# Kernel tuning notes

Hardware: AMD Instinct MI355X
Metric: run time of the kernel (lower is better)

Reference implementation:

```python
import jax, jax.numpy as jnp
import numpy as np

N_NODES = 100000


def gcn_conv(x, src, dst, W, b):
    # PyG GCNConv: add self-loops, symmetric norm D^-1/2 (A+I) D^-1/2, then linear.
    n = x.shape[0]
    xw = x @ W  # [N, out]
    deg = jax.ops.segment_sum(jnp.ones_like(dst, dtype=xw.dtype), dst, num_segments=n)
    dinv = jnp.where(deg > 0, jax.lax.rsqrt(deg), 0.0)
    norm = dinv[src] * dinv[dst]  # [E_total]
    out = jax.ops.segment_sum(norm[:, None] * xw[src], dst, num_segments=n)
    return out + b


def setup_inputs() -> dict:
    key = jax.random.key(0)
    k1, k2, k3, k4, k5, k6 = jax.random.split(key, 6)
    d = 64
    E = 1600000
    x = jax.random.normal(k1, (N_NODES, d), dtype=jnp.float32)
    edge_index = jax.random.randint(k2, (2, E), 0, N_NODES, dtype=jnp.int64)
    s = 1.0 / np.sqrt(d)
    W1 = jax.random.normal(k3, (d, d), dtype=jnp.float32) * s
    b1 = jax.random.normal(k4, (d,), dtype=jnp.float32) * 0.01
    W2 = jax.random.normal(k5, (d, d), dtype=jnp.float32) * s
    b2 = jax.random.normal(k6, (d,), dtype=jnp.float32) * 0.01
    return {"x": x, "edge_index": edge_index, "W1": W1, "b1": b1, "W2": W2, "b2": b2}


def reference(x, edge_index, W1, b1, W2, b2):
    n = x.shape[0]
    loops = jnp.arange(n, dtype=edge_index.dtype)
    src = jnp.concatenate([edge_index[0], loops])
    dst = jnp.concatenate([edge_index[1], loops])
    out = jax.nn.relu(gcn_conv(x, src, dst, W1, b1))
    out = gcn_conv(out, src, dst, W2, b2)
    return jax.nn.relu(out + x)
```

## Files before the change

kernel.cpp:

```cpp
#include <hip/hip_runtime.h>

constexpr int BIN_CHUNK = 2048;
constexpr int BK_SHIFT  = 9;
constexpr int BK_NODES  = 1 << BK_SHIFT;
constexpr int CAP       = 10240;

static __device__ __forceinline__ float4 mkf4(float x, float y, float z, float w) {
  float4 r; r.x = x; r.y = y; r.z = z; r.w = w; return r;
}

static __device__ __forceinline__ unsigned pack_bf16(float a, float b) {
  unsigned ua = __float_as_uint(a); ua = (ua + 0x7fffu + ((ua >> 16) & 1u)) >> 16;
  unsigned ub = __float_as_uint(b); ub = (ub + 0x7fffu + ((ub >> 16) & 1u)) >> 16;
  return ua | (ub << 16);
}
static __device__ __forceinline__ float blo(unsigned v) { return __uint_as_float(v << 16); }
static __device__ __forceinline__ float bhi(unsigned v) { return __uint_as_float(v & 0xffff0000u); }


__global__ void k_zero256(int* __restrict__ p) { p[threadIdx.x] = 0; }


__global__ __launch_bounds__(256) void k_bin(const int* __restrict__ src,
                                             const int* __restrict__ dst,
                                             int* __restrict__ bcur,
                                             int* __restrict__ binned, int E) {
  __shared__ int lh[4][256];
  __shared__ int cbase[4][256];
  const int tid = threadIdx.x, wv = tid >> 6, lane = tid & 63;
  for (int i = lane; i < 256; i += 64) lh[wv][i] = 0;
  __syncthreads();

  const int e0 = blockIdx.x * BIN_CHUNK;
  const int e1 = min(e0 + BIN_CHUNK, E);
  const int q  = BIN_CHUNK / 4;
  const int we0 = min(e0 + wv * q, e1);
  const int we1 = min(we0 + q, e1);

  for (int e = we0 + lane; e < we1; e += 64)
    atomicAdd(&lh[wv][dst[e] >> BK_SHIFT], 1);
  __syncthreads();

  {
    const int b = tid;
    int c0 = lh[0][b], c1 = lh[1][b], c2 = lh[2][b], c3 = lh[3][b];
    int tot = c0 + c1 + c2 + c3;
    int base = tot ? atomicAdd(bcur + b, tot) : 0;
    cbase[0][b] = base;
    cbase[1][b] = base + c0;
    cbase[2][b] = base + c0 + c1;
    cbase[3][b] = base + c0 + c1 + c2;
    lh[0][b] = 0; lh[1][b] = 0; lh[2][b] = 0; lh[3][b] = 0;
  }
  __syncthreads();

  for (int e = we0 + lane; e < we1; e += 64) {
    int d = dst[e];
    int b = d >> BK_SHIFT;
    int pos = cbase[wv][b] + atomicAdd(&lh[wv][b], 1);
    if (pos < CAP)
      binned[b * CAP + pos] = src[e] | ((d & (BK_NODES - 1)) << 17);
  }
}


__global__ __launch_bounds__(256) void k_place3(const int* __restrict__ bcur,
                                                const int* __restrict__ binned,
                                                int2* __restrict__ nfo,
                                                float* __restrict__ dinv,
                                                int* __restrict__ col, int N) {
  __shared__ int lhw[4][BK_NODES];
  __shared__ int lplace[CAP];
  __shared__ int wsum[4];
  const int tid = threadIdx.x, lane = tid & 63, wv = tid >> 6;
  const int b = blockIdx.x;
  const int nb0 = b << BK_SHIFT;
  const int base = b * CAP;
  const int len = min(bcur[b], CAP);

  for (int i = tid; i < 4 * BK_NODES; i += 256) ((int*)lhw)[i] = 0;
  __syncthreads();

  const int q = (len + 3) >> 2;
  const int we0 = min(wv * q, len);
  const int we1 = min(we0 + q, len);

  for (int e = we0 + lane; e < we1; e += 64)
    atomicAdd(&lhw[wv][binned[base + e] >> 17], 1);
  __syncthreads();

  const int i0 = 2 * tid, i1 = 2 * tid + 1;
  const int c0 = lhw[0][i0] + lhw[1][i0] + lhw[2][i0] + lhw[3][i0];
  const int c1 = lhw[0][i1] + lhw[1][i1] + lhw[2][i1] + lhw[3][i1];
  const int tot = c0 + c1;
  int t = tot;
#pragma unroll
  for (int o = 1; o < 64; o <<= 1) { int n = __shfl_up(t, o); if (lane >= o) t += n; }
  if (lane == 63) wsum[wv] = t;
  __syncthreads();
  int wbase = 0;
#pragma unroll
  for (int w = 0; w < 3; ++w) if (w < wv) wbase += wsum[w];
  const int excl = wbase + t - tot;

  const int n0 = nb0 + i0, n1 = nb0 + i1;
  if (n0 < N) {
    int2 s; s.x = base + excl; s.y = base + excl + c0;
    nfo[n0] = s; dinv[n0] = rsqrtf((float)(c0 + 1));
  }
  if (n1 < N) {
    int2 s; s.x = base + excl + c0; s.y = base + excl + c0 + c1;
    nfo[n1] = s; dinv[n1] = rsqrtf((float)(c1 + 1));
  }

  int run = excl;
#pragma unroll
  for (int w = 0; w < 4; ++w) { int tmp = lhw[w][i0]; lhw[w][i0] = run; run += tmp; }
#pragma unroll
  for (int w = 0; w < 4; ++w) { int tmp = lhw[w][i1]; lhw[w][i1] = run; run += tmp; }
  __syncthreads();

  for (int e = we0 + lane; e < we1; e += 64) {
    int v = binned[base + e];
    int pos = atomicAdd(&lhw[wv][v >> 17], 1);
    lplace[pos] = v & 0x1FFFF;
  }
  __syncthreads();
  for (int e = tid; e < len; e += 256) col[base + e] = lplace[e];
}


__global__ __launch_bounds__(256) void k_gemmf(const float* __restrict__ X,
                                               const float* __restrict__ W,
                                               const float* __restrict__ dinv,
                                               unsigned* __restrict__ Y, int N) {
  __shared__ float4 Wl[1024];
  const int tid = threadIdx.x;
  const float4* __restrict__ W4 = (const float4*)W;
#pragma unroll
  for (int i = 0; i < 4; ++i) Wl[tid + i * 256] = W4[tid + i * 256];
  __syncthreads();

  const int rg = tid >> 4, cq = tid & 15;
  const int row0 = blockIdx.x * 64 + rg * 4;
  const float4* __restrict__ X4 = (const float4*)X;

  int ridx[4];
#pragma unroll
  for (int r = 0; r < 4; ++r) ridx[r] = min(row0 + r, N - 1);

  float4 acc[4];
#pragma unroll
  for (int r = 0; r < 4; ++r) acc[r] = mkf4(0.f, 0.f, 0.f, 0.f);

#pragma unroll 4
  for (int k4 = 0; k4 < 16; ++k4) {
    float4 xv[4];
#pragma unroll
    for (int r = 0; r < 4; ++r) xv[r] = X4[(size_t)ridx[r] * 16 + k4];
#pragma unroll
    for (int kk = 0; kk < 4; ++kk) {
      const float4 w = Wl[(k4 * 4 + kk) * 16 + cq];
#pragma unroll
      for (int r = 0; r < 4; ++r) {
        const float xk = (kk == 0) ? xv[r].x : (kk == 1) ? xv[r].y
                        : (kk == 2) ? xv[r].z : xv[r].w;
        acc[r].x = fmaf(xk, w.x, acc[r].x);
        acc[r].y = fmaf(xk, w.y, acc[r].y);
        acc[r].z = fmaf(xk, w.z, acc[r].z);
        acc[r].w = fmaf(xk, w.w, acc[r].w);
      }
    }
  }

#pragma unroll
  for (int r = 0; r < 4; ++r) {
    const int row = row0 + r;
    if (row < N) {
      const float di = dinv[row];
      uint2 o;
      o.x = pack_bf16(di * acc[r].x, di * acc[r].y);
      o.y = pack_bf16(di * acc[r].z, di * acc[r].w);
      *(uint2*)(Y + (size_t)row * 32 + cq * 2) = o;
    }
  }
}


__global__ __launch_bounds__(256) void k_gemmb(const uint4* __restrict__ X4,
                                               const float* __restrict__ W,
                                               const float* __restrict__ dinv,
                                               unsigned* __restrict__ Y, int N) {
  __shared__ float4 Wl[1024];
  const int tid = threadIdx.x;
  const float4* __restrict__ W4 = (const float4*)W;
#pragma unroll
  for (int i = 0; i < 4; ++i) Wl[tid + i * 256] = W4[tid + i * 256];
  __syncthreads();

  const int rg = tid >> 4, cq = tid & 15;
  const int row0 = blockIdx.x * 64 + rg * 4;

  int ridx[4];
#pragma unroll
  for (int r = 0; r < 4; ++r) ridx[r] = min(row0 + r, N - 1);

  float4 acc[4];
#pragma unroll
  for (int r = 0; r < 4; ++r) acc[r] = mkf4(0.f, 0.f, 0.f, 0.f);

#pragma unroll 2
  for (int k8 = 0; k8 < 8; ++k8) {
    uint4 xv[4];
#pragma unroll
    for (int r = 0; r < 4; ++r) xv[r] = X4[(size_t)ridx[r] * 8 + k8];
#pragma unroll
    for (int kk = 0; kk < 8; ++kk) {
      const float4 w = Wl[(k8 * 8 + kk) * 16 + cq];
#pragma unroll
      for (int r = 0; r < 4; ++r) {
        const unsigned d = (kk < 2) ? xv[r].x : (kk < 4) ? xv[r].y
                          : (kk < 6) ? xv[r].z : xv[r].w;
        const float xk = (kk & 1) ? bhi(d) : blo(d);
        acc[r].x = fmaf(xk, w.x, acc[r].x);
        acc[r].y = fmaf(xk, w.y, acc[r].y);
        acc[r].z = fmaf(xk, w.z, acc[r].z);
        acc[r].w = fmaf(xk, w.w, acc[r].w);
      }
    }
  }

#pragma unroll
  for (int r = 0; r < 4; ++r) {
    const int row = row0 + r;
    if (row < N) {
      const float di = dinv[row];
      uint2 o;
      o.x = pack_bf16(di * acc[r].x, di * acc[r].y);
      o.y = pack_bf16(di * acc[r].z, di * acc[r].w);
      *(uint2*)(Y + (size_t)row * 32 + cq * 2) = o;
    }
  }
}


template <int MODE>
__global__ __launch_bounds__(256) void k_gather(const int2* __restrict__ nfo,
                                                const int* __restrict__ col,
                                                const float* __restrict__ dinv,
                                                const uint2* __restrict__ xws2,
                                                const float4* __restrict__ b4,
                                                const float4* __restrict__ x4,
                                                void* __restrict__ outp, int N) {
  const int node = blockIdx.x * 4 + (threadIdx.x >> 6);
  if (node >= N) return;
  const int lane = threadIdx.x & 63;
  const int sub = lane >> 4;
  const int lg = lane & 15;

  const int2 se = nfo[node];
  const uint2 sv = xws2[(size_t)node * 16 + lg];
  const float di = dinv[node];
  const float4 bb = b4[lg];
  float4 xx = mkf4(0.f, 0.f, 0.f, 0.f);
  if (MODE == 2) xx = x4[(size_t)node * 16 + lg];

  const int s0 = se.x;
  const int deg = se.y - se.x;
  const int dcap = min(deg, 64);

  int cv = 0;
  if (deg > 0) cv = col[min(s0 + lane, s0 + deg - 1)];

  float a0 = 0.f, a1 = 0.f, a2 = 0.f, a3 = 0.f;

  int jb = 0;
  for (; jb + 16 <= dcap; jb += 16) {
    int c0 = __shfl(cv, jb + sub);
    int c1 = __shfl(cv, jb + 4 + sub);
    int c2 = __shfl(cv, jb + 8 + sub);
    int c3 = __shfl(cv, jb + 12 + sub);
    uint2 v0 = xws2[(size_t)c0 * 16 + lg];
    uint2 v1 = xws2[(size_t)c1 * 16 + lg];
    uint2 v2 = xws2[(size_t)c2 * 16 + lg];
    uint2 v3 = xws2[(size_t)c3 * 16 + lg];
    a0 += (blo(v0.x) + blo(v1.x)) + (blo(v2.x) + blo(v3.x));
    a1 += (bhi(v0.x) + bhi(v1.x)) + (bhi(v2.x) + bhi(v3.x));
    a2 += (blo(v0.y) + blo(v1.y)) + (blo(v2.y) + blo(v3.y));
    a3 += (bhi(v0.y) + bhi(v1.y)) + (bhi(v2.y) + bhi(v3.y));
  }
  if (jb < dcap) {
    const int j0 = jb + sub, j1 = jb + 4 + sub, j2 = jb + 8 + sub, j3 = jb + 12 + sub;
    const int m = dcap - 1;
    int c0 = __shfl(cv, min(j0, m));
    int c1 = __shfl(cv, min(j1, m));
    int c2 = __shfl(cv, min(j2, m));
    int c3 = __shfl(cv, min(j3, m));
    uint2 v0 = xws2[(size_t)c0 * 16 + lg];
    uint2 v1 = xws2[(size_t)c1 * 16 + lg];
    uint2 v2 = xws2[(size_t)c2 * 16 + lg];
    uint2 v3 = xws2[(size_t)c3 * 16 + lg];
    a0 += (j0 < dcap ? blo(v0.x) : 0.f) + (j1 < dcap ? blo(v1.x) : 0.f)
        + (j2 < dcap ? blo(v2.x) : 0.f) + (j3 < dcap ? blo(v3.x) : 0.f);
    a1 += (j0 < dcap ? bhi(v0.x) : 0.f) + (j1 < dcap ? bhi(v1.x) : 0.f)
        + (j2 < dcap ? bhi(v2.x) : 0.f) + (j3 < dcap ? bhi(v3.x) : 0.f);
    a2 += (j0 < dcap ? blo(v0.y) : 0.f) + (j1 < dcap ? blo(v1.y) : 0.f)
        + (j2 < dcap ? blo(v2.y) : 0.f) + (j3 < dcap ? blo(v3.y) : 0.f);
    a3 += (j0 < dcap ? bhi(v0.y) : 0.f) + (j1 < dcap ? bhi(v1.y) : 0.f)
        + (j2 < dcap ? bhi(v2.y) : 0.f) + (j3 < dcap ? bhi(v3.y) : 0.f);
  }
  for (int e = s0 + 64 + sub; e < s0 + deg; e += 4) {
    uint2 v = xws2[(size_t)col[e] * 16 + lg];
    a0 += blo(v.x); a1 += bhi(v.x); a2 += blo(v.y); a3 += bhi(v.y);
  }

  a0 += __shfl_xor(a0, 16); a1 += __shfl_xor(a1, 16);
  a2 += __shfl_xor(a2, 16); a3 += __shfl_xor(a3, 16);
  a0 += __shfl_xor(a0, 32); a1 += __shfl_xor(a1, 32);
  a2 += __shfl_xor(a2, 32); a3 += __shfl_xor(a3, 32);

  if (sub == 0) {
    a0 += blo(sv.x); a1 += bhi(sv.x); a2 += blo(sv.y); a3 += bhi(sv.y);
    float r0 = fmaf(di, a0, bb.x);
    float r1 = fmaf(di, a1, bb.y);
    float r2 = fmaf(di, a2, bb.z);
    float r3 = fmaf(di, a3, bb.w);
    if (MODE == 2) {
      r0 += xx.x; r1 += xx.y; r2 += xx.z; r3 += xx.w;
      ((float4*)outp)[(size_t)node * 16 + lg] =
          mkf4(fmaxf(r0, 0.f), fmaxf(r1, 0.f), fmaxf(r2, 0.f), fmaxf(r3, 0.f));
    } else {
      uint2 o;
      o.x = pack_bf16(fmaxf(r0, 0.f), fmaxf(r1, 0.f));
      o.y = pack_bf16(fmaxf(r2, 0.f), fmaxf(r3, 0.f));
      ((uint2*)outp)[(size_t)node * 16 + lg] = o;
    }
  }
}


extern "C" void kernel_launch(void* const* d_in, const int* in_sizes, int n_in,
                              void* d_out, int out_size, void* d_ws, size_t ws_size,
                              hipStream_t stream) {
  const float* x  = (const float*)d_in[0];
  const int*   ei = (const int*)d_in[1];
  const float* W1 = (const float*)d_in[2];
  const float* b1 = (const float*)d_in[3];
  const float* W2 = (const float*)d_in[4];
  const float* b2 = (const float*)d_in[5];
  float* out = (float*)d_out;

  const int N = in_sizes[0] / 64;
  const int E = in_sizes[1] / 2;
  const int NB = (N + BK_NODES - 1) >> BK_SHIFT;

  const int* srcp = ei;
  const int* dstp = ei + E;

  auto align = [](size_t v) { return (v + 255) & ~(size_t)255; };
  char* ws = (char*)d_ws;
  size_t o = 0;
  int2* nfo   = (int2*)(ws + o); o = align(o + (size_t)N * 8);
  float* dinv = (float*)(ws + o); o = align(o + (size_t)N * 4);
  int* bcur   = (int*)(ws + o); o = align(o + 256 * 4);
  int* col    = (int*)(ws + o); o = align(o + (size_t)NB * CAP * 4);
  unsigned* xws = (unsigned*)(ws + o); o = align(o + (size_t)N * 128);
  unsigned* h1  = (unsigned*)(ws + o); o = align(o + (size_t)N * 128);
  int* binned = (int*)h1;

  const int bGm  = (N + 63) / 64;
  const int bG   = (N + 3) / 4;
  const int bBin = (E + BIN_CHUNK - 1) / BIN_CHUNK;

  k_zero256<<<1, 256, 0, stream>>>(bcur);
  k_bin<<<bBin, 256, 0, stream>>>(srcp, dstp, bcur, binned, E);
  k_place3<<<NB, 256, 0, stream>>>(bcur, binned, nfo, dinv, col, N);

  k_gemmf<<<bGm, 256, 0, stream>>>(x, W1, dinv, xws, N);
  k_gather<1><<<bG, 256, 0, stream>>>(nfo, col, dinv, (const uint2*)xws,
                                      (const float4*)b1, (const float4*)x,
                                      (void*)h1, N);

  k_gemmb<<<bGm, 256, 0, stream>>>((const uint4*)h1, W2, dinv, xws, N);
  k_gather<2><<<bG, 256, 0, stream>>>(nfo, col, dinv, (const uint2*)xws,
                                      (const float4*)b2, (const float4*)x,
                                      (void*)out, N);
}
```

Measured before the change: 173.1 us.

## Halve bucket size, vectorize binning loads, packed-float gather accumulation

Buckets shrink from 512 to 256 nodes (CAP 5120, up to 512 buckets), so k_place3 launches twice as many blocks with one node per thread and a smaller LDS footprint, which should raise occupancy. k_bin reads dst/src as int4 when the chunk is full and aligned, the col copy-out uses int4 stores, and the gather accumulates bf16 pairs in 2-wide float vectors to encourage packed FP32 adds. The smaller CAP leaves less headroom for skewed bucket sizes, and more buckets raises contention on the global bucket counters.

```diff
diff --git a/kernel.cpp b/kernel.cpp
--- a/kernel.cpp
+++ b/kernel.cpp
@@ -1,9 +1,12 @@
 #include <hip/hip_runtime.h>
 
 constexpr int BIN_CHUNK = 2048;
-constexpr int BK_SHIFT  = 9;
+constexpr int BK_SHIFT  = 8;
 constexpr int BK_NODES  = 1 << BK_SHIFT;
-constexpr int CAP       = 10240;
+constexpr int NBMAX     = 512;
+constexpr int CAP       = 5120;
+
+typedef float v2f __attribute__((ext_vector_type(2)));
 
 static __device__ __forceinline__ float4 mkf4(float x, float y, float z, float w) {
   float4 r; r.x = x; r.y = y; r.z = z; r.w = w; return r;
@@ -16,19 +19,22 @@
 }
 static __device__ __forceinline__ float blo(unsigned v) { return __uint_as_float(v << 16); }
 static __device__ __forceinline__ float bhi(unsigned v) { return __uint_as_float(v & 0xffff0000u); }
-
-
-__global__ void k_zero256(int* __restrict__ p) { p[threadIdx.x] = 0; }
+static __device__ __forceinline__ v2f bpair(unsigned v) {
+  v2f p; p.x = blo(v); p.y = bhi(v); return p;
+}
+
+
+__global__ void k_zero(int* __restrict__ p) { p[threadIdx.x] = 0; }
 
 
 __global__ __launch_bounds__(256) void k_bin(const int* __restrict__ src,
                                              const int* __restrict__ dst,
                                              int* __restrict__ bcur,
                                              int* __restrict__ binned, int E) {
-  __shared__ int lh[4][256];
-  __shared__ int cbase[4][256];
+  __shared__ int lh[4][NBMAX];
+  __shared__ int cbase[4][NBMAX];
   const int tid = threadIdx.x, wv = tid >> 6, lane = tid & 63;
-  for (int i = lane; i < 256; i += 64) lh[wv][i] = 0;
+  for (int i = lane; i < NBMAX; i += 64) lh[wv][i] = 0;
   __syncthreads();
 
   const int e0 = blockIdx.x * BIN_CHUNK;
@@ -36,13 +42,26 @@
   const int q  = BIN_CHUNK / 4;
   const int we0 = min(e0 + wv * q, e1);
   const int we1 = min(we0 + q, e1);
-
-  for (int e = we0 + lane; e < we1; e += 64)
-    atomicAdd(&lh[wv][dst[e] >> BK_SHIFT], 1);
-  __syncthreads();
-
-  {
-    const int b = tid;
+  const bool vec = (we1 - we0 == q) &&
+                   (((((size_t)(dst + we0)) | ((size_t)(src + we0))) & 15) == 0);
+
+  if (vec) {
+    const int4* __restrict__ d4 = (const int4*)(dst + we0);
+#pragma unroll
+    for (int j = 0; j < 2; ++j) {
+      int4 d = d4[lane + j * 64];
+      atomicAdd(&lh[wv][d.x >> BK_SHIFT], 1);
+      atomicAdd(&lh[wv][d.y >> BK_SHIFT], 1);
+      atomicAdd(&lh[wv][d.z >> BK_SHIFT], 1);
+      atomicAdd(&lh[wv][d.w >> BK_SHIFT], 1);
+    }
+  } else {
+    for (int e = we0 + lane; e < we1; e += 64)
+      atomicAdd(&lh[wv][dst[e] >> BK_SHIFT], 1);
+  }
+  __syncthreads();
+
+  for (int b = tid; b < NBMAX; b += 256) {
     int c0 = lh[0][b], c1 = lh[1][b], c2 = lh[2][b], c3 = lh[3][b];
     int tot = c0 + c1 + c2 + c3;
     int base = tot ? atomicAdd(bcur + b, tot) : 0;
@@ -54,12 +73,30 @@
   }
   __syncthreads();
 
-  for (int e = we0 + lane; e < we1; e += 64) {
-    int d = dst[e];
-    int b = d >> BK_SHIFT;
-    int pos = cbase[wv][b] + atomicAdd(&lh[wv][b], 1);
-    if (pos < CAP)
-      binned[b * CAP + pos] = src[e] | ((d & (BK_NODES - 1)) << 17);
+  if (vec) {
+    const int4* __restrict__ d4 = (const int4*)(dst + we0);
+    const int4* __restrict__ s4 = (const int4*)(src + we0);
+#pragma unroll
+    for (int j = 0; j < 2; ++j) {
+      int4 d = d4[lane + j * 64];
+      int4 s = s4[lane + j * 64];
+      int b, pos;
+      b = d.x >> BK_SHIFT; pos = cbase[wv][b] + atomicAdd(&lh[wv][b], 1);
+      if (pos < CAP) binned[b * CAP + pos] = s.x | ((d.x & (BK_NODES - 1)) << 17);
+      b = d.y >> BK_SHIFT; pos = cbase[wv][b] + atomicAdd(&lh[wv][b], 1);
+      if (pos < CAP) binned[b * CAP + pos] = s.y | ((d.y & (BK_NODES - 1)) << 17);
+      b = d.z >> BK_SHIFT; pos = cbase[wv][b] + atomicAdd(&lh[wv][b], 1);
+      if (pos < CAP) binned[b * CAP + pos] = s.z | ((d.z & (BK_NODES - 1)) << 17);
+      b = d.w >> BK_SHIFT; pos = cbase[wv][b] + atomicAdd(&lh[wv][b], 1);
+      if (pos < CAP) binned[b * CAP + pos] = s.w | ((d.w & (BK_NODES - 1)) << 17);
+    }
+  } else {
+    for (int e = we0 + lane; e < we1; e += 64) {
+      int d = dst[e];
+      int b = d >> BK_SHIFT;
+      int pos = cbase[wv][b] + atomicAdd(&lh[wv][b], 1);
+      if (pos < CAP) binned[b * CAP + pos] = src[e] | ((d & (BK_NODES - 1)) << 17);
+    }
   }
 }
 
@@ -78,7 +115,8 @@
   const int base = b * CAP;
   const int len = min(bcur[b], CAP);
 
-  for (int i = tid; i < 4 * BK_NODES; i += 256) ((int*)lhw)[i] = 0;
+#pragma unroll
+  for (int i = 0; i < 4; ++i) ((int*)lhw)[tid + i * 256] = 0;
   __syncthreads();
 
   const int q = (len + 3) >> 2;
@@ -89,11 +127,8 @@
     atomicAdd(&lhw[wv][binned[base + e] >> 17], 1);
   __syncthreads();
 
-  const int i0 = 2 * tid, i1 = 2 * tid + 1;
-  const int c0 = lhw[0][i0] + lhw[1][i0] + lhw[2][i0] + lhw[3][i0];
-  const int c1 = lhw[0][i1] + lhw[1][i1] + lhw[2][i1] + lhw[3][i1];
-  const int tot = c0 + c1;
-  int t = tot;
+  const int c = lhw[0][tid] + lhw[1][tid] + lhw[2][tid] + lhw[3][tid];
+  int t = c;
 #pragma unroll
   for (int o = 1; o < 64; o <<= 1) { int n = __shfl_up(t, o); if (lane >= o) t += n; }
   if (lane == 63) wsum[wv] = t;
@@ -101,23 +136,18 @@
   int wbase = 0;
 #pragma unroll
   for (int w = 0; w < 3; ++w) if (w < wv) wbase += wsum[w];
-  const int excl = wbase + t - tot;
-
-  const int n0 = nb0 + i0, n1 = nb0 + i1;
-  if (n0 < N) {
-    int2 s; s.x = base + excl; s.y = base + excl + c0;
-    nfo[n0] = s; dinv[n0] = rsqrtf((float)(c0 + 1));
-  }
-  if (n1 < N) {
-    int2 s; s.x = base + excl + c0; s.y = base + excl + c0 + c1;
-    nfo[n1] = s; dinv[n1] = rsqrtf((float)(c1 + 1));
+  const int excl = wbase + t - c;
+
+  const int node = nb0 + tid;
+  if (node < N) {
+    int2 s; s.x = base + excl; s.y = base + excl + c;
+    nfo[node] = s;
+    dinv[node] = rsqrtf((float)(c + 1));
   }
 
   int run = excl;
 #pragma unroll
-  for (int w = 0; w < 4; ++w) { int tmp = lhw[w][i0]; lhw[w][i0] = run; run += tmp; }
-#pragma unroll
-  for (int w = 0; w < 4; ++w) { int tmp = lhw[w][i1]; lhw[w][i1] = run; run += tmp; }
+  for (int w = 0; w < 4; ++w) { int tmp = lhw[w][tid]; lhw[w][tid] = run; run += tmp; }
   __syncthreads();
 
   for (int e = we0 + lane; e < we1; e += 64) {
@@ -126,7 +156,12 @@
     lplace[pos] = v & 0x1FFFF;
   }
   __syncthreads();
-  for (int e = tid; e < len; e += 256) col[base + e] = lplace[e];
+
+  const int n4 = len >> 2;
+  int4* __restrict__ c4 = (int4*)(col + base);
+  const int4* __restrict__ p4 = (const int4*)lplace;
+  for (int i = tid; i < n4; i += 256) c4[i] = p4[i];
+  for (int e = (n4 << 2) + tid; e < len; e += 256) col[base + e] = lplace[e];
 }
 
 
@@ -272,7 +307,7 @@
   int cv = 0;
   if (deg > 0) cv = col[min(s0 + lane, s0 + deg - 1)];
 
-  float a0 = 0.f, a1 = 0.f, a2 = 0.f, a3 = 0.f;
+  v2f A0 = (v2f)0.f, A1 = (v2f)0.f;
 
   int jb = 0;
   for (; jb + 16 <= dcap; jb += 16) {
@@ -284,10 +319,8 @@
     uint2 v1 = xws2[(size_t)c1 * 16 + lg];
     uint2 v2 = xws2[(size_t)c2 * 16 + lg];
     uint2 v3 = xws2[(size_t)c3 * 16 + lg];
-    a0 += (blo(v0.x) + blo(v1.x)) + (blo(v2.x) + blo(v3.x));
-    a1 += (bhi(v0.x) + bhi(v1.x)) + (bhi(v2.x) + bhi(v3.x));
-    a2 += (blo(v0.y) + blo(v1.y)) + (blo(v2.y) + blo(v3.y));
-    a3 += (bhi(v0.y) + bhi(v1.y)) + (bhi(v2.y) + bhi(v3.y));
+    A0 += (bpair(v0.x) + bpair(v1.x)) + (bpair(v2.x) + bpair(v3.x));
+    A1 += (bpair(v0.y) + bpair(v1.y)) + (bpair(v2.y) + bpair(v3.y));
   }
   if (jb < dcap) {
     const int j0 = jb + sub, j1 = jb + 4 + sub, j2 = jb + 8 + sub, j3 = jb + 12 + sub;
@@ -300,20 +333,18 @@
     uint2 v1 = xws2[(size_t)c1 * 16 + lg];
     uint2 v2 = xws2[(size_t)c2 * 16 + lg];
     uint2 v3 = xws2[(size_t)c3 * 16 + lg];
-    a0 += (j0 < dcap ? blo(v0.x) : 0.f) + (j1 < dcap ? blo(v1.x) : 0.f)
-        + (j2 < dcap ? blo(v2.x) : 0.f) + (j3 < dcap ? blo(v3.x) : 0.f);
-    a1 += (j0 < dcap ? bhi(v0.x) : 0.f) + (j1 < dcap ? bhi(v1.x) : 0.f)
-        + (j2 < dcap ? bhi(v2.x) : 0.f) + (j3 < dcap ? bhi(v3.x) : 0.f);
-    a2 += (j0 < dcap ? blo(v0.y) : 0.f) + (j1 < dcap ? blo(v1.y) : 0.f)
-        + (j2 < dcap ? blo(v2.y) : 0.f) + (j3 < dcap ? blo(v3.y) : 0.f);
-    a3 += (j0 < dcap ? bhi(v0.y) : 0.f) + (j1 < dcap ? bhi(v1.y) : 0.f)
-        + (j2 < dcap ? bhi(v2.y) : 0.f) + (j3 < dcap ? bhi(v3.y) : 0.f);
+    const v2f z = (v2f)0.f;
+    A0 += (j0 < dcap ? bpair(v0.x) : z) + (j1 < dcap ? bpair(v1.x) : z)
+        + (j2 < dcap ? bpair(v2.x) : z) + (j3 < dcap ? bpair(v3.x) : z);
+    A1 += (j0 < dcap ? bpair(v0.y) : z) + (j1 < dcap ? bpair(v1.y) : z)
+        + (j2 < dcap ? bpair(v2.y) : z) + (j3 < dcap ? bpair(v3.y) : z);
   }
   for (int e = s0 + 64 + sub; e < s0 + deg; e += 4) {
     uint2 v = xws2[(size_t)col[e] * 16 + lg];
-    a0 += blo(v.x); a1 += bhi(v.x); a2 += blo(v.y); a3 += bhi(v.y);
-  }
-
+    A0 += bpair(v.x); A1 += bpair(v.y);
+  }
+
+  float a0 = A0.x, a1 = A0.y, a2 = A1.x, a3 = A1.y;
   a0 += __shfl_xor(a0, 16); a1 += __shfl_xor(a1, 16);
   a2 += __shfl_xor(a2, 16); a3 += __shfl_xor(a3, 16);
   a0 += __shfl_xor(a0, 32); a1 += __shfl_xor(a1, 32);
@@ -362,7 +393,7 @@
   size_t o = 0;
   int2* nfo   = (int2*)(ws + o); o = align(o + (size_t)N * 8);
   float* dinv = (float*)(ws + o); o = align(o + (size_t)N * 4);
-  int* bcur   = (int*)(ws + o); o = align(o + 256 * 4);
+  int* bcur   = (int*)(ws + o); o = align(o + NBMAX * 4);
   int* col    = (int*)(ws + o); o = align(o + (size_t)NB * CAP * 4);
   unsigned* xws = (unsigned*)(ws + o); o = align(o + (size_t)N * 128);
   unsigned* h1  = (unsigned*)(ws + o); o = align(o + (size_t)N * 128);
@@ -372,7 +403,7 @@
   const int bG   = (N + 3) / 4;
   const int bBin = (E + BIN_CHUNK - 1) / BIN_CHUNK;
 
-  k_zero256<<<1, 256, 0, stream>>>(bcur);
+  k_zero<<<1, NBMAX, 0, stream>>>(bcur);
   k_bin<<<bBin, 256, 0, stream>>>(srcp, dstp, bcur, binned, E);
   k_place3<<<NB, 256, 0, stream>>>(bcur, binned, nfo, dinv, col, N);
 
```

After: 169.6 us. -2.0%, faster.
